# Kernel tuning notes

Measured on AMD Instinct MI355X. Metric: run time of the kernel, lower is better.

The kernel has to match this reference:

```python
import jax, jax.numpy as jnp
import numpy as np

N_WITHIN = 20   # n_labels for active dataset (cityscapes)
N_CROSS = 27    # n_labels for other dataset (idd)
ALPHA = 0.5
BETA = 0.5
T = 1.0


def _l2norm_rows(w):
    return w / jnp.sqrt(jnp.sum(w * w, axis=1, keepdims=True) + 1e-12)


def setup_inputs() -> dict:
    key = jax.random.key(0)
    k1, k2, k3, k4 = jax.random.split(key, 4)
    B, D, H, W = 4, 64, 512, 512
    encoder_op = jax.random.normal(k1, (B, D, H, W), jnp.float32)
    # conv weights are row-normalized label embeddings (frozen in original)
    w_within = _l2norm_rows(jax.random.normal(k2, (N_WITHIN, D), jnp.float32))
    w_cross = _l2norm_rows(jax.random.normal(k3, (N_CROSS, D), jnp.float32))
    targets = jax.random.randint(k4, (B, H, W), 0, N_WITHIN, dtype=jnp.int32)
    return {"encoder_op": encoder_op, "w_within": w_within,
            "w_cross": w_cross, "targets": targets}


def _entropy_loss(logits):
    # mean over (b,h,w) of -sum_c p * log p, softmax over channel dim 1
    logp = jax.nn.log_softmax(logits, axis=1)
    p = jnp.exp(logp)
    return jnp.mean(-jnp.sum(p * logp, axis=1)).reshape(-1)


def reference(encoder_op, w_within, w_cross, targets):
    # 1x1 conv == channel contraction; drop last (background) channel as in torch code
    within_map = jnp.einsum('bdhw,nd->bnhw', encoder_op, w_within)[:, :-1]
    cross_map = jnp.einsum('bdhw,nd->bnhw', encoder_op, w_cross)[:, :-1] / T
    loss_unsup = ALPHA * _entropy_loss(cross_map) + BETA * _entropy_loss(within_map)

    # _update_centroids: per-label masked sum == segment_sum over flattened pixels
    B, D, H, W = encoder_op.shape
    feats = encoder_op.transpose(0, 2, 3, 1).reshape(-1, D)  # [B*H*W, D]
    labs = targets.reshape(-1)                               # [B*H*W]
    centroids = jax.ops.segment_sum(feats, labs, num_segments=N_WITHIN)  # [N, D]
    counts = jax.ops.segment_sum(jnp.ones_like(labs, dtype=jnp.int32), labs,
                                 num_segments=N_WITHIN)                   # [N]
    # original detaches centroids (.data)
    return loss_unsup, jax.lax.stop_gradient(centroids), counts
```

## Files before the change

kernel.cpp:

```cpp
#include <hip/hip_runtime.h>
#include <hip/hip_bf16.h>

#define HW_   (512 * 512)
#define B_    4
#define D_    64
#define NPIX  (B_ * HW_)
#define NW    19
#define NC    26
#define NLAB  45
#define NSEG  20
#define WSTRIDE 48
#define THREADS 256

#define LW(X)  X(0)X(1)X(2)X(3)X(4)X(5)X(6)X(7)X(8)X(9)X(10)X(11)X(12)X(13)X(14)X(15)X(16)X(17)X(18)
#define LC(X)  X(19)X(20)X(21)X(22)X(23)X(24)X(25)X(26)X(27)X(28)X(29)X(30)X(31)X(32)X(33)X(34)X(35)X(36)X(37)X(38)X(39)X(40)X(41)X(42)X(43)X(44)
#define LA(X)  LW(X) LC(X)

__global__ void transpose_w(const float* __restrict__ wW, const float* __restrict__ wC,
                            float* __restrict__ wT) {
    int i = blockIdx.x * 256 + threadIdx.x;
    if (i < D_ * NLAB) {
        int c = i / NLAB, n = i - c * NLAB;
        wT[c * WSTRIDE + n] = (n < NW) ? wW[n * D_ + c] : wC[(n - NW) * D_ + c];
    }
}

__global__ __launch_bounds__(THREADS)
__attribute__((amdgpu_waves_per_eu(6, 6)))
void fused_embed(const float* __restrict__ enc, const float* __restrict__ wT,
                 const int* __restrict__ targ, float* __restrict__ out)
{
    __shared__ float sCent[NSEG][D_ + 1];
    __shared__ int   sCount[NSEG];
    __shared__ float sRed[THREADS / 64];

    const int tid = threadIdx.x;
    for (int i = tid; i < NSEG * (D_ + 1); i += THREADS) (&sCent[0][0])[i] = 0.f;
    if (tid < NSEG) sCount[tid] = 0;
    __syncthreads();

    const int p   = blockIdx.x * THREADS + tid;
    const int b   = (blockIdx.x * THREADS) / HW_;
    const int hw0 = p - b * HW_;
    const float* fp = enc + (size_t)b * (D_ * HW_) + hw0;
    const int lab = targ[p];

#define DECL_ACC(n) float a##n = 0.f;
    LA(DECL_ACC)
#undef DECL_ACC

    float fcur = fp[0];
#pragma unroll 1
    for (int c = 0; c < D_ - 1; ++c) {
        float fnext = fp[(size_t)(c + 1) * HW_];
        const float* wr = wT + c * WSTRIDE;
#define FMA1(n) a##n = fmaf(fcur, wr[n], a##n);
        LA(FMA1)
#undef FMA1
        atomicAdd(&sCent[lab][c], fcur);
        fcur = fnext;
    }
    {
        const float* wr = wT + (D_ - 1) * WSTRIDE;
#define FMA1(n) a##n = fmaf(fcur, wr[n], a##n);
        LA(FMA1)
#undef FMA1
        atomicAdd(&sCent[lab][D_ - 1], fcur);
    }
    atomicAdd(&sCount[lab], 1);

    float lossAcc;
    {
        float S = 0.f, Wt = 0.f;
#define ES(n) { float e = __expf(a##n); S += e; Wt = fmaf(e, a##n, Wt); }
        LW(ES)
#undef ES
        lossAcc = __logf(S) - Wt / S;
    }
    {
        float S = 0.f, Wt = 0.f;
#define ES(n) { float e = __expf(a##n); S += e; Wt = fmaf(e, a##n, Wt); }
        LC(ES)
#undef ES
        lossAcc += __logf(S) - Wt / S;
    }

#pragma unroll
    for (int off = 32; off; off >>= 1) lossAcc += __shfl_down(lossAcc, off);
    if ((tid & 63) == 0) sRed[tid >> 6] = lossAcc;
    __syncthreads();
    if (tid == 0) {
        float s = 0.f;
#pragma unroll
        for (int w = 0; w < THREADS / 64; ++w) s += sRed[w];
        atomicAdd(out, s * (0.5f / (float)NPIX));
    }

    for (int i = tid; i < NSEG * D_; i += THREADS) {
        int n = i >> 6, d = i & 63;
        atomicAdd(&out[1 + i], sCent[n][d]);
    }
    if (tid < NSEG) atomicAdd(&out[1 + NSEG * D_ + tid], (float)sCount[tid]);
}

extern "C" void kernel_launch(void* const* d_in, const int* in_sizes, int n_in,
                              void* d_out, int out_size, void* d_ws, size_t ws_size,
                              hipStream_t stream) {
    const float* enc = (const float*)d_in[0];
    const float* wW  = (const float*)d_in[1];
    const float* wC  = (const float*)d_in[2];
    const int*   targ = (const int*)d_in[3];
    float* out = (float*)d_out;
    float* wT  = (float*)d_ws;

    hipMemsetAsync(d_out, 0, (size_t)out_size * sizeof(float), stream);

    transpose_w<<<dim3((D_ * NLAB + 255) / 256), dim3(256), 0, stream>>>(wW, wC, wT);
    fused_embed<<<dim3(NPIX / THREADS), dim3(THREADS), 0, stream>>>(enc, wT, targ, out);
}
```

Baseline: 444.0 us.

## Split projection into two passes over channels to cut live accumulators

```diff
diff --git a/kernel.cpp b/kernel.cpp
--- a/kernel.cpp
+++ b/kernel.cpp
@@ -7,29 +7,36 @@
 #define NPIX  (B_ * HW_)
 #define NW    19
 #define NC    26
-#define NLAB  45
 #define NSEG  20
-#define WSTRIDE 48
+#define SW_   20
+#define SC_   28
 #define THREADS 256
 
-#define LW(X)  X(0)X(1)X(2)X(3)X(4)X(5)X(6)X(7)X(8)X(9)X(10)X(11)X(12)X(13)X(14)X(15)X(16)X(17)X(18)
-#define LC(X)  X(19)X(20)X(21)X(22)X(23)X(24)X(25)X(26)X(27)X(28)X(29)X(30)X(31)X(32)X(33)X(34)X(35)X(36)X(37)X(38)X(39)X(40)X(41)X(42)X(43)X(44)
-#define LA(X)  LW(X) LC(X)
+#define L19(X) X(0)X(1)X(2)X(3)X(4)X(5)X(6)X(7)X(8)X(9)X(10)X(11)X(12)X(13)X(14)X(15)X(16)X(17)X(18)
+#define L26(X) X(0)X(1)X(2)X(3)X(4)X(5)X(6)X(7)X(8)X(9)X(10)X(11)X(12)X(13)X(14)X(15)X(16)X(17)X(18)X(19)X(20)X(21)X(22)X(23)X(24)X(25)
 
 __global__ void transpose_w(const float* __restrict__ wW, const float* __restrict__ wC,
-                            float* __restrict__ wT) {
+                            float* __restrict__ ws) {
     int i = blockIdx.x * 256 + threadIdx.x;
-    if (i < D_ * NLAB) {
-        int c = i / NLAB, n = i - c * NLAB;
-        wT[c * WSTRIDE + n] = (n < NW) ? wW[n * D_ + c] : wC[(n - NW) * D_ + c];
+    float* wTW = ws;
+    float* wTC = ws + D_ * SW_;
+    if (i < D_ * SW_) {
+        int c = i / SW_, n = i - c * SW_;
+        wTW[i] = (n < NW) ? wW[n * D_ + c] : 0.f;
+    }
+    if (i < D_ * SC_) {
+        int c = i / SC_, n = i - c * SC_;
+        wTC[i] = (n < NC) ? wC[n * D_ + c] : 0.f;
     }
 }
 
 __global__ __launch_bounds__(THREADS)
-__attribute__((amdgpu_waves_per_eu(6, 6)))
-void fused_embed(const float* __restrict__ enc, const float* __restrict__ wT,
+void fused_embed(const float* __restrict__ enc, const float* __restrict__ ws,
                  const int* __restrict__ targ, float* __restrict__ out)
 {
+    const float* wTW = ws;
+    const float* wTC = ws + D_ * SW_;
+
     __shared__ float sCent[NSEG][D_ + 1];
     __shared__ int   sCount[NSEG];
     __shared__ float sRed[THREADS / 64];
@@ -45,42 +52,50 @@
     const float* fp = enc + (size_t)b * (D_ * HW_) + hw0;
     const int lab = targ[p];
 
-#define DECL_ACC(n) float a##n = 0.f;
-    LA(DECL_ACC)
-#undef DECL_ACC
+    float lossAcc = 0.f;
 
-    float fcur = fp[0];
+    {
+#define DECL(n) float a##n = 0.f;
+        L19(DECL)
+#undef DECL
 #pragma unroll 1
-    for (int c = 0; c < D_ - 1; ++c) {
-        float fnext = fp[(size_t)(c + 1) * HW_];
-        const float* wr = wT + c * WSTRIDE;
-#define FMA1(n) a##n = fmaf(fcur, wr[n], a##n);
-        LA(FMA1)
-#undef FMA1
-        atomicAdd(&sCent[lab][c], fcur);
-        fcur = fnext;
-    }
-    {
-        const float* wr = wT + (D_ - 1) * WSTRIDE;
-#define FMA1(n) a##n = fmaf(fcur, wr[n], a##n);
-        LA(FMA1)
-#undef FMA1
-        atomicAdd(&sCent[lab][D_ - 1], fcur);
-    }
-    atomicAdd(&sCount[lab], 1);
+        for (int c = 0; c < D_; c += 2) {
+            float f0 = fp[(size_t)c * HW_];
+            float f1 = fp[(size_t)(c + 1) * HW_];
+            const float* r0 = wTW + c * SW_;
+            const float* r1 = r0 + SW_;
+#define FMA2(n) { a##n = fmaf(r0[n], f0, a##n); a##n = fmaf(r1[n], f1, a##n); }
+            L19(FMA2)
+#undef FMA2
+            atomicAdd(&sCent[lab][c], f0);
+            atomicAdd(&sCent[lab][c + 1], f1);
+        }
+        atomicAdd(&sCount[lab], 1);
 
-    float lossAcc;
-    {
         float S = 0.f, Wt = 0.f;
 #define ES(n) { float e = __expf(a##n); S += e; Wt = fmaf(e, a##n, Wt); }
-        LW(ES)
+        L19(ES)
 #undef ES
-        lossAcc = __logf(S) - Wt / S;
+        lossAcc += __logf(S) - Wt / S;
     }
+
     {
+#define DECL(n) float a##n = 0.f;
+        L26(DECL)
+#undef DECL
+#pragma unroll 1
+        for (int c = 0; c < D_; c += 2) {
+            float f0 = fp[(size_t)c * HW_];
+            float f1 = fp[(size_t)(c + 1) * HW_];
+            const float* r0 = wTC + c * SC_;
+            const float* r1 = r0 + SC_;
+#define FMA2(n) { a##n = fmaf(r0[n], f0, a##n); a##n = fmaf(r1[n], f1, a##n); }
+            L26(FMA2)
+#undef FMA2
+        }
         float S = 0.f, Wt = 0.f;
 #define ES(n) { float e = __expf(a##n); S += e; Wt = fmaf(e, a##n, Wt); }
-        LC(ES)
+        L26(ES)
 #undef ES
         lossAcc += __logf(S) - Wt / S;
     }
@@ -111,10 +126,10 @@
     const float* wC  = (const float*)d_in[2];
     const int*   targ = (const int*)d_in[3];
     float* out = (float*)d_out;
-    float* wT  = (float*)d_ws;
+    float* ws  = (float*)d_ws;
 
     hipMemsetAsync(d_out, 0, (size_t)out_size * sizeof(float), stream);
 
-    transpose_w<<<dim3((D_ * NLAB + 255) / 256), dim3(256), 0, stream>>>(wW, wC, wT);
-    fused_embed<<<dim3(NPIX / THREADS), dim3(THREADS), 0, stream>>>(enc, wT, targ, out);
+    transpose_w<<<dim3((D_ * SC_ + 255) / 256), dim3(256), 0, stream>>>(wW, wC, ws);
+    fused_embed<<<dim3(NPIX / THREADS), dim3(THREADS), 0, stream>>>(enc, ws, targ, out);
 }
```

New measurement: 380.5 us. 14.3% less time.

## Compute label logits with bf16 MFMA via swizzled LDS tiles, 8 tiles per block

Applied to the files above, without the earlier changes.

```diff
diff --git a/kernel.cpp b/kernel.cpp
--- a/kernel.cpp
+++ b/kernel.cpp
@@ -1,98 +1,153 @@
 #include <hip/hip_runtime.h>
-#include <hip/hip_bf16.h>
+
+typedef short short8 __attribute__((ext_vector_type(8)));
+typedef float f32x4 __attribute__((ext_vector_type(4)));
 
 #define HW_   (512 * 512)
 #define B_    4
 #define D_    64
 #define NPIX  (B_ * HW_)
 #define NW    19
-#define NC    26
 #define NLAB  45
 #define NSEG  20
-#define WSTRIDE 48
 #define THREADS 256
+#define TILES 8
+#define BLKPIX (THREADS * TILES)
+#define NBLK  (NPIX / BLKPIX)
 
-#define LW(X)  X(0)X(1)X(2)X(3)X(4)X(5)X(6)X(7)X(8)X(9)X(10)X(11)X(12)X(13)X(14)X(15)X(16)X(17)X(18)
-#define LC(X)  X(19)X(20)X(21)X(22)X(23)X(24)X(25)X(26)X(27)X(28)X(29)X(30)X(31)X(32)X(33)X(34)X(35)X(36)X(37)X(38)X(39)X(40)X(41)X(42)X(43)X(44)
-#define LA(X)  LW(X) LC(X)
+__device__ __forceinline__ unsigned short f2bf(float x) {
+    unsigned u = __float_as_uint(x);
+    return (unsigned short)((u + 0x7FFFu + ((u >> 16) & 1u)) >> 16);
+}
 
-__global__ void transpose_w(const float* __restrict__ wW, const float* __restrict__ wC,
-                            float* __restrict__ wT) {
-    int i = blockIdx.x * 256 + threadIdx.x;
-    if (i < D_ * NLAB) {
-        int c = i / NLAB, n = i - c * NLAB;
-        wT[c * WSTRIDE + n] = (n < NW) ? wW[n * D_ + c] : wC[(n - NW) * D_ + c];
+__global__ void prep_b(const float* __restrict__ wW, const float* __restrict__ wC,
+                       unsigned short* __restrict__ wsB) {
+    int tid = threadIdx.x;
+    for (int kk = 0; kk < 12; ++kk) {
+        int idx = tid + kk * 256;
+        int q = idx >> 9, rem = idx & 511;
+        int l = rem >> 3, j = rem & 7;
+        int col = (q >> 1) * 16 + (l & 15);
+        int kch = (q & 1) * 32 + ((l >> 4) * 8) + j;
+        float v = 0.f;
+        if (col < NW) v = wW[col * D_ + kch];
+        else if (col < NLAB) v = wC[(col - NW) * D_ + kch];
+        wsB[idx] = f2bf(v);
     }
 }
 
 __global__ __launch_bounds__(THREADS)
-__attribute__((amdgpu_waves_per_eu(6, 6)))
-void fused_embed(const float* __restrict__ enc, const float* __restrict__ wT,
+void fused_embed(const float* __restrict__ enc, const unsigned short* __restrict__ wsB,
                  const int* __restrict__ targ, float* __restrict__ out)
 {
+    __shared__ short sF[THREADS * D_];
     __shared__ float sCent[NSEG][D_ + 1];
     __shared__ int   sCount[NSEG];
-    __shared__ float sRed[THREADS / 64];
+    __shared__ float sRed[4];
 
-    const int tid = threadIdx.x;
+    const int tid  = threadIdx.x;
+    const int lane = tid & 63, w = tid >> 6;
+    const int l15  = lane & 15, g = lane >> 4;
+
     for (int i = tid; i < NSEG * (D_ + 1); i += THREADS) (&sCent[0][0])[i] = 0.f;
     if (tid < NSEG) sCount[tid] = 0;
+
+    short8 b00 = *(const short8*)&wsB[(0 * 64 + lane) * 8];
+    short8 b01 = *(const short8*)&wsB[(1 * 64 + lane) * 8];
+    short8 b10 = *(const short8*)&wsB[(2 * 64 + lane) * 8];
+    short8 b11 = *(const short8*)&wsB[(3 * 64 + lane) * 8];
+    short8 b20 = *(const short8*)&wsB[(4 * 64 + lane) * 8];
+    short8 b21 = *(const short8*)&wsB[(5 * 64 + lane) * 8];
+
+    const int blk0 = blockIdx.x * BLKPIX;
+    const int b    = blk0 / HW_;
+    float lossAcc = 0.f;
     __syncthreads();
 
-    const int p   = blockIdx.x * THREADS + tid;
-    const int b   = (blockIdx.x * THREADS) / HW_;
-    const int hw0 = p - b * HW_;
-    const float* fp = enc + (size_t)b * (D_ * HW_) + hw0;
-    const int lab = targ[p];
+    for (int t8 = 0; t8 < TILES; ++t8) {
+        const int p = blk0 + t8 * THREADS + tid;
+        const float* fpx = enc + (size_t)b * D_ * HW_ + (p - b * HW_);
+        const int lab = targ[p];
 
-#define DECL_ACC(n) float a##n = 0.f;
-    LA(DECL_ACC)
-#undef DECL_ACC
+#pragma unroll 2
+        for (int c0 = 0; c0 < D_; c0 += 8) {
+            float g0 = fpx[(size_t)(c0 + 0) * HW_];
+            float g1 = fpx[(size_t)(c0 + 1) * HW_];
+            float g2 = fpx[(size_t)(c0 + 2) * HW_];
+            float g3 = fpx[(size_t)(c0 + 3) * HW_];
+            float g4 = fpx[(size_t)(c0 + 4) * HW_];
+            float g5 = fpx[(size_t)(c0 + 5) * HW_];
+            float g6 = fpx[(size_t)(c0 + 6) * HW_];
+            float g7 = fpx[(size_t)(c0 + 7) * HW_];
+            atomicAdd(&sCent[lab][c0 + 0], g0);
+            atomicAdd(&sCent[lab][c0 + 1], g1);
+            atomicAdd(&sCent[lab][c0 + 2], g2);
+            atomicAdd(&sCent[lab][c0 + 3], g3);
+            atomicAdd(&sCent[lab][c0 + 4], g4);
+            atomicAdd(&sCent[lab][c0 + 5], g5);
+            atomicAdd(&sCent[lab][c0 + 6], g6);
+            atomicAdd(&sCent[lab][c0 + 7], g7);
+            short8 v;
+            v[0] = (short)f2bf(g0); v[1] = (short)f2bf(g1);
+            v[2] = (short)f2bf(g2); v[3] = (short)f2bf(g3);
+            v[4] = (short)f2bf(g4); v[5] = (short)f2bf(g5);
+            v[6] = (short)f2bf(g6); v[7] = (short)f2bf(g7);
+            *(short8*)&sF[(tid << 6) + ((((c0 >> 3) ^ (tid & 7))) << 3)] = v;
+        }
+        atomicAdd(&sCount[lab], 1);
+        __syncthreads();
 
-    float fcur = fp[0];
-#pragma unroll 1
-    for (int c = 0; c < D_ - 1; ++c) {
-        float fnext = fp[(size_t)(c + 1) * HW_];
-        const float* wr = wT + c * WSTRIDE;
-#define FMA1(n) a##n = fmaf(fcur, wr[n], a##n);
-        LA(FMA1)
-#undef FMA1
-        atomicAdd(&sCent[lab][c], fcur);
-        fcur = fnext;
-    }
-    {
-        const float* wr = wT + (D_ - 1) * WSTRIDE;
-#define FMA1(n) a##n = fmaf(fcur, wr[n], a##n);
-        LA(FMA1)
-#undef FMA1
-        atomicAdd(&sCent[lab][D_ - 1], fcur);
-    }
-    atomicAdd(&sCount[lab], 1);
+        f32x4 a00 = {0,0,0,0}, a01 = {0,0,0,0}, a02 = {0,0,0,0};
+        f32x4 a10 = {0,0,0,0}, a11 = {0,0,0,0}, a12 = {0,0,0,0};
+        f32x4 a20 = {0,0,0,0}, a21 = {0,0,0,0}, a22 = {0,0,0,0};
+        f32x4 a30 = {0,0,0,0}, a31 = {0,0,0,0}, a32 = {0,0,0,0};
 
-    float lossAcc;
-    {
-        float S = 0.f, Wt = 0.f;
-#define ES(n) { float e = __expf(a##n); S += e; Wt = fmaf(e, a##n, Wt); }
-        LW(ES)
-#undef ES
-        lossAcc = __logf(S) - Wt / S;
-    }
-    {
-        float S = 0.f, Wt = 0.f;
-#define ES(n) { float e = __expf(a##n); S += e; Wt = fmaf(e, a##n, Wt); }
-        LC(ES)
-#undef ES
-        lossAcc += __logf(S) - Wt / S;
+#define MSTEP(m, A0, A1, A2) { \
+        const int pr = (w << 6) + ((m) << 4) + l15;   \
+        short8 af0 = *(const short8*)&sF[(pr << 6) + (((g)     ^ (l15 & 7)) << 3)]; \
+        short8 af1 = *(const short8*)&sF[(pr << 6) + (((4 + g) ^ (l15 & 7)) << 3)]; \
+        A0 = __builtin_amdgcn_mfma_f32_16x16x32_bf16(af0, b00, A0, 0, 0, 0); \
+        A0 = __builtin_amdgcn_mfma_f32_16x16x32_bf16(af1, b01, A0, 0, 0, 0); \
+        A1 = __builtin_amdgcn_mfma_f32_16x16x32_bf16(af0, b10, A1, 0, 0, 0); \
+        A1 = __builtin_amdgcn_mfma_f32_16x16x32_bf16(af1, b11, A1, 0, 0, 0); \
+        A2 = __builtin_amdgcn_mfma_f32_16x16x32_bf16(af0, b20, A2, 0, 0, 0); \
+        A2 = __builtin_amdgcn_mfma_f32_16x16x32_bf16(af1, b21, A2, 0, 0, 0); }
+        MSTEP(0, a00, a01, a02)
+        MSTEP(1, a10, a11, a12)
+        MSTEP(2, a20, a21, a22)
+        MSTEP(3, a30, a31, a32)
+#undef MSTEP
+
+#define ENTROPY(A0, A1, A2) { \
+        _Pragma("unroll") \
+        for (int i = 0; i < 4; ++i) { \
+            float x0 = A0[i], x1 = A1[i], x2 = A2[i]; \
+            float e0 = __expf(x0), e1 = __expf(x1), e2 = __expf(x2); \
+            bool w1 = (l15 < 3), v2 = (l15 < 13); \
+            float sw = e0 + (w1 ? e1 : 0.f); \
+            float ww = x0 * e0 + (w1 ? x1 * e1 : 0.f); \
+            float sc = (w1 ? 0.f : e1) + (v2 ? e2 : 0.f); \
+            float wc = (w1 ? 0.f : x1 * e1) + (v2 ? x2 * e2 : 0.f); \
+            _Pragma("unroll") \
+            for (int off = 1; off < 16; off <<= 1) { \
+                sw += __shfl_xor(sw, off, 16); ww += __shfl_xor(ww, off, 16); \
+                sc += __shfl_xor(sc, off, 16); wc += __shfl_xor(wc, off, 16); } \
+            if (l15 == 0) lossAcc += (__logf(sw) - ww / sw) + (__logf(sc) - wc / sc); \
+        } }
+        ENTROPY(a00, a01, a02)
+        ENTROPY(a10, a11, a12)
+        ENTROPY(a20, a21, a22)
+        ENTROPY(a30, a31, a32)
+#undef ENTROPY
+        __syncthreads();
     }
 
 #pragma unroll
     for (int off = 32; off; off >>= 1) lossAcc += __shfl_down(lossAcc, off);
-    if ((tid & 63) == 0) sRed[tid >> 6] = lossAcc;
+    if (lane == 0) sRed[w] = lossAcc;
     __syncthreads();
     if (tid == 0) {
-        float s = 0.f;
-#pragma unroll
-        for (int w = 0; w < THREADS / 64; ++w) s += sRed[w];
+        float s = sRed[0] + sRed[1] + sRed[2] + sRed[3];
         atomicAdd(out, s * (0.5f / (float)NPIX));
     }
 
@@ -111,10 +166,10 @@
     const float* wC  = (const float*)d_in[2];
     const int*   targ = (const int*)d_in[3];
     float* out = (float*)d_out;
-    float* wT  = (float*)d_ws;
+    unsigned short* wsB = (unsigned short*)d_ws;
 
     hipMemsetAsync(d_out, 0, (size_t)out_size * sizeof(float), stream);
 
-    transpose_w<<<dim3((D_ * NLAB + 255) / 256), dim3(256), 0, stream>>>(wW, wC, wT);
-    fused_embed<<<dim3(NPIX / THREADS), dim3(THREADS), 0, stream>>>(enc, wT, targ, out);
+    prep_b<<<dim3(1), dim3(256), 0, stream>>>(wW, wC, wsB);
+    fused_embed<<<dim3(NBLK), dim3(THREADS), 0, stream>>>(enc, wsB, targ, out);
 }
```

Measured after the change: 428.1 us. 1.04x faster.

## Split label logits across four waves per pixel tile and merge softmax sums

Applied to the files above, without the earlier changes.

```diff
diff --git a/kernel.cpp b/kernel.cpp
--- a/kernel.cpp
+++ b/kernel.cpp
@@ -1,5 +1,4 @@
 #include <hip/hip_runtime.h>
-#include <hip/hip_bf16.h>
 
 #define HW_   (512 * 512)
 #define B_    4
@@ -7,93 +6,93 @@
 #define NPIX  (B_ * HW_)
 #define NW    19
 #define NC    26
-#define NLAB  45
 #define NSEG  20
-#define WSTRIDE 48
 #define THREADS 256
+#define TILES 8
+#define BLKPIX 512
+#define NBLK  (NPIX / BLKPIX)
+#define WSTR  16
 
-#define LW(X)  X(0)X(1)X(2)X(3)X(4)X(5)X(6)X(7)X(8)X(9)X(10)X(11)X(12)X(13)X(14)X(15)X(16)X(17)X(18)
-#define LC(X)  X(19)X(20)X(21)X(22)X(23)X(24)X(25)X(26)X(27)X(28)X(29)X(30)X(31)X(32)X(33)X(34)X(35)X(36)X(37)X(38)X(39)X(40)X(41)X(42)X(43)X(44)
-#define LA(X)  LW(X) LC(X)
+#define L13(X) X(0)X(1)X(2)X(3)X(4)X(5)X(6)X(7)X(8)X(9)X(10)X(11)X(12)
 
-__global__ void transpose_w(const float* __restrict__ wW, const float* __restrict__ wC,
-                            float* __restrict__ wT) {
+__global__ void prep_w(const float* __restrict__ wW, const float* __restrict__ wC,
+                       float* __restrict__ ws) {
     int i = blockIdx.x * 256 + threadIdx.x;
-    if (i < D_ * NLAB) {
-        int c = i / NLAB, n = i - c * NLAB;
-        wT[c * WSTRIDE + n] = (n < NW) ? wW[n * D_ + c] : wC[(n - NW) * D_ + c];
+    if (i < 4 * D_ * WSTR) {
+        int w = i >> 10, rem = i & 1023, c = rem >> 4, idx = rem & 15;
+        float v = 0.f;
+        if      (w == 0) { if (idx < 10) v = wW[idx * D_ + c]; }
+        else if (w == 1) { if (idx < 9)  v = wW[(10 + idx) * D_ + c]; }
+        else if (w == 2) { if (idx < 13) v = wC[idx * D_ + c]; }
+        else             { if (idx < 13) v = wC[(13 + idx) * D_ + c]; }
+        ws[i] = v;
     }
 }
 
 __global__ __launch_bounds__(THREADS)
-__attribute__((amdgpu_waves_per_eu(6, 6)))
-void fused_embed(const float* __restrict__ enc, const float* __restrict__ wT,
+void fused_embed(const float* __restrict__ enc, const float* __restrict__ ws,
                  const int* __restrict__ targ, float* __restrict__ out)
 {
     __shared__ float sCent[NSEG][D_ + 1];
     __shared__ int   sCount[NSEG];
-    __shared__ float sRed[THREADS / 64];
+    __shared__ float sS[4 * 64], sWt[4 * 64];
 
-    const int tid = threadIdx.x;
+    const int tid  = threadIdx.x;
+    const int lane = tid & 63, w = tid >> 6;
+
     for (int i = tid; i < NSEG * (D_ + 1); i += THREADS) (&sCent[0][0])[i] = 0.f;
     if (tid < NSEG) sCount[tid] = 0;
     __syncthreads();
 
-    const int p   = blockIdx.x * THREADS + tid;
-    const int b   = (blockIdx.x * THREADS) / HW_;
-    const int hw0 = p - b * HW_;
-    const float* fp = enc + (size_t)b * (D_ * HW_) + hw0;
-    const int lab = targ[p];
+    const int blk0 = blockIdx.x * BLKPIX;
+    const int b    = blk0 / HW_;
+    const float* wsb = ws + (w << 10);
+    const float nneg = (w == 0) ? 3.f : (w == 1) ? 4.f : 0.f;
+    float lossAcc = 0.f;
 
-#define DECL_ACC(n) float a##n = 0.f;
-    LA(DECL_ACC)
-#undef DECL_ACC
+    for (int t = 0; t < TILES; ++t) {
+        const int pt = blk0 + t * 64;
+        const float* fb = enc + (size_t)b * D_ * HW_ + (pt - b * HW_) + lane;
 
-    float fcur = fp[0];
+        float S = -nneg, Wt = 0.f;
+#define DECL(n) float a##n = 0.f;
+        L13(DECL)
+#undef DECL
 #pragma unroll 1
-    for (int c = 0; c < D_ - 1; ++c) {
-        float fnext = fp[(size_t)(c + 1) * HW_];
-        const float* wr = wT + c * WSTRIDE;
-#define FMA1(n) a##n = fmaf(fcur, wr[n], a##n);
-        LA(FMA1)
+        for (int c = 0; c < D_; ++c) {
+            float f = fb[(size_t)c * HW_];
+            const float* wr = wsb + (c << 4);
+#define FMA1(n) a##n = fmaf(wr[n], f, a##n);
+            L13(FMA1)
 #undef FMA1
-        atomicAdd(&sCent[lab][c], fcur);
-        fcur = fnext;
-    }
-    {
-        const float* wr = wT + (D_ - 1) * WSTRIDE;
-#define FMA1(n) a##n = fmaf(fcur, wr[n], a##n);
-        LA(FMA1)
-#undef FMA1
-        atomicAdd(&sCent[lab][D_ - 1], fcur);
-    }
-    atomicAdd(&sCount[lab], 1);
+        }
+#define ES(n) { float e = __expf(a##n); S += e; Wt = fmaf(e, a##n, Wt); }
+        L13(ES)
+#undef ES
+        sS[(w << 6) + lane] = S;  sWt[(w << 6) + lane] = Wt;
 
-    float lossAcc;
-    {
-        float S = 0.f, Wt = 0.f;
-#define ES(n) { float e = __expf(a##n); S += e; Wt = fmaf(e, a##n, Wt); }
-        LW(ES)
-#undef ES
-        lossAcc = __logf(S) - Wt / S;
-    }
-    {
-        float S = 0.f, Wt = 0.f;
-#define ES(n) { float e = __expf(a##n); S += e; Wt = fmaf(e, a##n, Wt); }
-        LC(ES)
-#undef ES
-        lossAcc += __logf(S) - Wt / S;
+        if (w == 0) {
+            const int lab = targ[pt + lane];
+#pragma unroll 8
+            for (int c = 0; c < D_; ++c)
+                atomicAdd(&sCent[lab][c], fb[(size_t)c * HW_]);
+            atomicAdd(&sCount[lab], 1);
+        }
+        __syncthreads();
+        if (w == 0) {
+            float Sw = sS[lane]       + sS[64 + lane];
+            float Ww = sWt[lane]      + sWt[64 + lane];
+            float Sc = sS[128 + lane] + sS[192 + lane];
+            float Wc = sWt[128 + lane] + sWt[192 + lane];
+            lossAcc += (__logf(Sw) - Ww / Sw) + (__logf(Sc) - Wc / Sc);
+        }
+        __syncthreads();
     }
 
+    if (w == 0) {
 #pragma unroll
-    for (int off = 32; off; off >>= 1) lossAcc += __shfl_down(lossAcc, off);
-    if ((tid & 63) == 0) sRed[tid >> 6] = lossAcc;
-    __syncthreads();
-    if (tid == 0) {
-        float s = 0.f;
-#pragma unroll
-        for (int w = 0; w < THREADS / 64; ++w) s += sRed[w];
-        atomicAdd(out, s * (0.5f / (float)NPIX));
+        for (int off = 32; off; off >>= 1) lossAcc += __shfl_down(lossAcc, off);
+        if (lane == 0) atomicAdd(out, lossAcc * (0.5f / (float)NPIX));
     }
 
     for (int i = tid; i < NSEG * D_; i += THREADS) {
@@ -111,10 +110,10 @@
     const float* wC  = (const float*)d_in[2];
     const int*   targ = (const int*)d_in[3];
     float* out = (float*)d_out;
-    float* wT  = (float*)d_ws;
+    float* ws  = (float*)d_ws;
 
     hipMemsetAsync(d_out, 0, (size_t)out_size * sizeof(float), stream);
 
-    transpose_w<<<dim3((D_ * NLAB + 255) / 256), dim3(256), 0, stream>>>(wW, wC, wT);
-    fused_embed<<<dim3(NPIX / THREADS), dim3(THREADS), 0, stream>>>(enc, wT, targ, out);
+    prep_w<<<dim3(16), dim3(256), 0, stream>>>(wW, wC, ws);
+    fused_embed<<<dim3(NBLK), dim3(THREADS), 0, stream>>>(enc, ws, targ, out);
 }
```

Measured after the change: 619.8 us. 39.6% more time.
